# Kernel tuning notes

Measured on AMD Instinct MI355X. Metric: run time of the kernel, lower is better.

Reference implementation:

```python
import jax, jax.numpy as jnp
import numpy as np

NUM_KNOTS = 10
NUM_PARAMS = 1


def setup_inputs() -> dict:
    key = jax.random.key(0)
    kx, _ = jax.random.split(key)
    x = jax.random.normal(kx, (16, 4096, 1024), dtype=jnp.float32)
    # learned parameters per init_kwargs (knots is unused in forward math)
    coeffs = jnp.ones((NUM_KNOTS, NUM_PARAMS), dtype=jnp.float32)
    return {"x": x, "coeffs": coeffs}


def reference(x, coeffs):
    # Original: expand x to [N, F, K], bmm with coeffs [K, P] -> [N, F, P],
    # reshape to [..., F*P], sum over last dim.
    # Since every knot-copy of x is identical:
    #   out[...] = (sum_f x[..., f]) * (sum_{k,p} coeffs[k, p])
    return x.sum(axis=-1) * coeffs.sum()
```

## Files before the change

kernel.cpp:

```cpp
#include <hip/hip_runtime.h>


#define F_DIM 1024
#define ROWS_PER_BLOCK 4

__global__ __launch_bounds__(256) void spline_rowsum_kernel(
    const float* __restrict__ x,
    const float* __restrict__ coeffs,
    float* __restrict__ out,
    long long nrows) {
  const int wave = threadIdx.x >> 6;
  const int lane = threadIdx.x & 63;
  const long long row = (long long)blockIdx.x * ROWS_PER_BLOCK + wave;
  if (row >= nrows) return;

  const float4* __restrict__ xr =
      reinterpret_cast<const float4*>(x + row * (long long)F_DIM);

  float s = 0.0f;
#pragma unroll
  for (int j = 0; j < 4; ++j) {
    float4 v = xr[j * 64 + lane];
    s += (v.x + v.y) + (v.z + v.w);
  }

#pragma unroll
  for (int off = 32; off > 0; off >>= 1)
    s += __shfl_down(s, off, 64);

  if (lane == 0) {
    float cs = 0.0f;
#pragma unroll
    for (int k = 0; k < 10; ++k) cs += coeffs[k];
    out[row] = s * cs;
  }
}

extern "C" void kernel_launch(void* const* d_in, const int* in_sizes, int n_in,
                              void* d_out, int out_size, void* d_ws, size_t ws_size,
                              hipStream_t stream) {
  const float* x      = (const float*)d_in[0];
  const float* coeffs = (const float*)d_in[1];
  float* out          = (float*)d_out;

  const long long nrows = (long long)out_size;
  const int blocks = (int)((nrows + ROWS_PER_BLOCK - 1) / ROWS_PER_BLOCK);
  spline_rowsum_kernel<<<blocks, 256, 0, stream>>>(x, coeffs, out, nrows);
}
```

Baseline: 346.9 us.

## Use persistent grid-stride waves with two rows in flight and nontemporal loads

Replaces one-row-per-wave blocks with a fixed grid of 2048 blocks whose waves stride over rows, processing two rows per iteration so eight 16-byte loads are outstanding at once. Loads use nontemporal hints to avoid polluting caches on a pure streaming read, and the coefficient sum is hoisted out of the per-row path. This aims to raise memory-level parallelism and cut block launch overhead on a bandwidth-bound 256MB reduction, at the cost of a fixed grid size that may underfill or unevenly balance the GPU.

```diff
diff --git a/kernel.cpp b/kernel.cpp
--- a/kernel.cpp
+++ b/kernel.cpp
@@ -1,38 +1,65 @@
 #include <hip/hip_runtime.h>
 
 
-#define F_DIM 1024
-#define ROWS_PER_BLOCK 4
+typedef float vf4 __attribute__((ext_vector_type(4)));
+
+#define WAVES_PER_BLOCK 4
+#define NUM_BLOCKS 2048
 
 __global__ __launch_bounds__(256) void spline_rowsum_kernel(
     const float* __restrict__ x,
     const float* __restrict__ coeffs,
     float* __restrict__ out,
-    long long nrows) {
-  const int wave = threadIdx.x >> 6;
+    int nrows) {
   const int lane = threadIdx.x & 63;
-  const long long row = (long long)blockIdx.x * ROWS_PER_BLOCK + wave;
-  if (row >= nrows) return;
+  const int w = blockIdx.x * WAVES_PER_BLOCK + (threadIdx.x >> 6);
+  const int total_waves = NUM_BLOCKS * WAVES_PER_BLOCK;
 
-  const float4* __restrict__ xr =
-      reinterpret_cast<const float4*>(x + row * (long long)F_DIM);
+  float cs = 0.0f;
+#pragma unroll
+  for (int k = 0; k < 10; ++k) cs += coeffs[k];
 
-  float s = 0.0f;
-#pragma unroll
-  for (int j = 0; j < 4; ++j) {
-    float4 v = xr[j * 64 + lane];
-    s += (v.x + v.y) + (v.z + v.w);
-  }
+  int r = w;
+  for (; r + total_waves < nrows; r += 2 * total_waves) {
+    const vf4* xa = reinterpret_cast<const vf4*>(x + (long long)r * 1024) + lane;
+    const vf4* xb = reinterpret_cast<const vf4*>(
+                        x + (long long)(r + total_waves) * 1024) + lane;
+
+    vf4 a0 = __builtin_nontemporal_load(xa + 0 * 64);
+    vf4 a1 = __builtin_nontemporal_load(xa + 1 * 64);
+    vf4 a2 = __builtin_nontemporal_load(xa + 2 * 64);
+    vf4 a3 = __builtin_nontemporal_load(xa + 3 * 64);
+    vf4 b0 = __builtin_nontemporal_load(xb + 0 * 64);
+    vf4 b1 = __builtin_nontemporal_load(xb + 1 * 64);
+    vf4 b2 = __builtin_nontemporal_load(xb + 2 * 64);
+    vf4 b3 = __builtin_nontemporal_load(xb + 3 * 64);
+
+    float sa = ((a0.x + a0.y) + (a0.z + a0.w)) + ((a1.x + a1.y) + (a1.z + a1.w))
+             + ((a2.x + a2.y) + (a2.z + a2.w)) + ((a3.x + a3.y) + (a3.z + a3.w));
+    float sb = ((b0.x + b0.y) + (b0.z + b0.w)) + ((b1.x + b1.y) + (b1.z + b1.w))
+             + ((b2.x + b2.y) + (b2.z + b2.w)) + ((b3.x + b3.y) + (b3.z + b3.w));
 
 #pragma unroll
-  for (int off = 32; off > 0; off >>= 1)
-    s += __shfl_down(s, off, 64);
-
-  if (lane == 0) {
-    float cs = 0.0f;
+    for (int off = 32; off > 0; off >>= 1) {
+      sa += __shfl_down(sa, off, 64);
+      sb += __shfl_down(sb, off, 64);
+    }
+    if (lane == 0) {
+      out[r] = sa * cs;
+      out[r + total_waves] = sb * cs;
+    }
+  }
+  if (r < nrows) {
+    const vf4* xa = reinterpret_cast<const vf4*>(x + (long long)r * 1024) + lane;
+    vf4 a0 = __builtin_nontemporal_load(xa + 0 * 64);
+    vf4 a1 = __builtin_nontemporal_load(xa + 1 * 64);
+    vf4 a2 = __builtin_nontemporal_load(xa + 2 * 64);
+    vf4 a3 = __builtin_nontemporal_load(xa + 3 * 64);
+    float sa = ((a0.x + a0.y) + (a0.z + a0.w)) + ((a1.x + a1.y) + (a1.z + a1.w))
+             + ((a2.x + a2.y) + (a2.z + a2.w)) + ((a3.x + a3.y) + (a3.z + a3.w));
 #pragma unroll
-    for (int k = 0; k < 10; ++k) cs += coeffs[k];
-    out[row] = s * cs;
+    for (int off = 32; off > 0; off >>= 1) sa += __shfl_down(sa, off, 64);
+    if (lane == 0) out[r] = sa * cs;
   }
 }
 
@@ -43,7 +70,5 @@
   const float* coeffs = (const float*)d_in[1];
   float* out          = (float*)d_out;
 
-  const long long nrows = (long long)out_size;
-  const int blocks = (int)((nrows + ROWS_PER_BLOCK - 1) / ROWS_PER_BLOCK);
-  spline_rowsum_kernel<<<blocks, 256, 0, stream>>>(x, coeffs, out, nrows);
+  spline_rowsum_kernel<<<NUM_BLOCKS, 256, 0, stream>>>(x, coeffs, out, out_size);
 }
```

Result: faster. 329.4 us (-5.0%).
